# Kernel tuning notes

Measured on AMD Instinct MI355X. Metric: run time of the kernel, lower is better.

Reference implementation:

```python
import jax, jax.numpy as jnp
import numpy as np

NSAMPLE = 32
LAMBDA = 0.5


def setup_inputs() -> dict:
    key = jax.random.key(0)
    k1, k2, k3, k4, k5 = jax.random.split(key, 5)
    B, N, NPOINT, C, NCOMP = 4, 8192, 2048, 64, 16
    xyz = jax.random.normal(k1, (B, N, 3), dtype=jnp.float32)
    new_xyz = jax.random.normal(k2, (B, NPOINT, 3), dtype=jnp.float32)
    components = jax.random.randint(k3, (B, N, 1), 0, NCOMP, dtype=jnp.int64)
    new_components = jax.random.randint(k4, (B, NPOINT, 1), 0, NCOMP, dtype=jnp.int64)
    features = jax.random.normal(k5, (B, C, N), dtype=jnp.float32)
    return {"xyz": xyz, "new_xyz": new_xyz, "components": components,
            "new_components": new_components, "features": features}


def _gag_knn(new_xyz, xyz, new_comp, comp, k, lam):
    # squared pairwise distances (B, npoint, N), same math as sum((src-dst)**2)
    diff = new_xyz[:, :, None, :] - xyz[:, None, :, :]
    dists = jnp.sum(diff * diff, axis=-1)
    # component-aware rescale
    mask = comp[:, None, :] == new_comp[:, :, None]  # (B, npoint, N)
    dists = jnp.where(mask, dists * lam, dists * (1.0 - lam))
    # full argsort then take first k (faithful to original)
    idx = jnp.argsort(dists, axis=-1)[:, :, :k]  # (B, npoint, k)
    return idx.astype(jnp.int32)


def reference(xyz, new_xyz, components, new_components, features):
    comp = components[..., 0]
    new_comp = new_components[..., 0]
    idx = _gag_knn(new_xyz, xyz, new_comp, comp, NSAMPLE, LAMBDA)  # (B, npoint, ns)

    # group xyz: gather along N -> (B, npoint, ns, 3)
    grouped_xyz = jnp.take_along_axis(xyz[:, None, :, :], idx[..., None], axis=2)
    grouped_xyz = grouped_xyz - new_xyz[:, :, None, :]
    grouped_xyz = jnp.transpose(grouped_xyz, (0, 3, 1, 2))  # (B, 3, npoint, ns)

    # group features: (B, C, N) -> (B, npoint, ns, C) -> (B, C, npoint, ns)
    feats_bnc = jnp.transpose(features, (0, 2, 1))  # (B, N, C)
    grouped_feats = jnp.take_along_axis(feats_bnc[:, None, :, :], idx[..., None], axis=2)
    grouped_feats = jnp.transpose(grouped_feats, (0, 3, 1, 2))  # (B, C, npoint, ns)

    return jnp.concatenate([grouped_xyz, grouped_feats], axis=1)  # (B, 3+C, npoint, ns)
```

## Files before the change

kernel.cpp:

```cpp
#include <hip/hip_runtime.h>


#define BQ 4
#define NN_ 8192
#define NPOINT 2048
#define CF 64
#define NS 32
#define T1 256
#define PER (NN_ / T1)
#define CAP 1024

__global__ __launch_bounds__(256) void knn_kernel(const float* __restrict__ xyz,
                                                  const float* __restrict__ new_xyz,
                                                  int* __restrict__ idxOut) {
  const int q = blockIdx.x;
  const int b = q / NPOINT;
  const int tid = threadIdx.x;

  const float qx = new_xyz[q * 3 + 0];
  const float qy = new_xyz[q * 3 + 1];
  const float qz = new_xyz[q * 3 + 2];

  const float* __restrict__ base = xyz + (size_t)b * NN_ * 3;

  float d[PER];
  float lmin = 3.4e38f;
  int n = tid;
#pragma unroll
  for (int j = 0; j < PER; j++, n += T1) {
    float dx = base[n * 3 + 0] - qx;
    float dy = base[n * 3 + 1] - qy;
    float dz = base[n * 3 + 2] - qz;
    float dist = __fadd_rn(__fadd_rn(__fmul_rn(dx, dx), __fmul_rn(dy, dy)),
                           __fmul_rn(dz, dz));
    dist *= 0.5f;
    d[j] = dist;
    lmin = fminf(lmin, dist);
  }

  __shared__ float mins[T1];
  mins[tid] = lmin;
  __syncthreads();
  for (int k = 2; k <= T1; k <<= 1) {
    for (int j = k >> 1; j > 0; j >>= 1) {
      int ixj = tid ^ j;
      if (ixj > tid) {
        float a = mins[tid], bb = mins[ixj];
        bool up = ((tid & k) == 0);
        if (up ? (a > bb) : (a < bb)) { mins[tid] = bb; mins[ixj] = a; }
      }
      __syncthreads();
    }
  }
  const float theta = mins[NS - 1];

  __shared__ unsigned long long cand[CAP];
  __shared__ int cnt;
  if (tid == 0) cnt = 0;
  __syncthreads();
  n = tid;
#pragma unroll
  for (int j = 0; j < PER; j++, n += T1) {
    if (d[j] <= theta) {
      int pos = atomicAdd(&cnt, 1);
      if (pos < CAP)
        cand[pos] = ((unsigned long long)__float_as_uint(d[j]) << 32) | (unsigned)n;
    }
  }
  __syncthreads();
  int m = cnt < CAP ? cnt : CAP;

  for (int i = tid; i < m; i += T1) {
    unsigned long long x = cand[i];
    int r = 0;
    for (int j = 0; j < m; j++) r += (cand[j] < x) ? 1 : 0;
    if (r < NS) idxOut[q * NS + r] = (int)(x & 0xffffffffu);
  }
}

__global__ __launch_bounds__(256) void transpose_kernel(const float* __restrict__ f,
                                                        float* __restrict__ ft) {
  __shared__ float t[32][33];
  const int b = blockIdx.z;
  const int n0 = blockIdx.x * 32;
  const int c0 = blockIdx.y * 32;
  const int tx = threadIdx.x;
  const int ty = threadIdx.y;
#pragma unroll
  for (int i = 0; i < 4; i++) {
    int c = c0 + ty + i * 8;
    t[ty + i * 8][tx] = f[(size_t)b * CF * NN_ + (size_t)c * NN_ + n0 + tx];
  }
  __syncthreads();
#pragma unroll
  for (int i = 0; i < 4; i++) {
    int nrow = n0 + ty + i * 8;
    ft[(size_t)b * NN_ * CF + (size_t)nrow * CF + c0 + tx] = t[tx][ty + i * 8];
  }
}

#define FSTR 68
__global__ __launch_bounds__(256) void group_kernel(const float* __restrict__ xyz,
                                                    const float* __restrict__ new_xyz,
                                                    const float* __restrict__ featsT,
                                                    const int* __restrict__ idxArr,
                                                    float* __restrict__ out) {
  const int q = blockIdx.x;
  const int b = q / NPOINT;
  const int p = q - b * NPOINT;
  const int tid = threadIdx.x;

  __shared__ int sIdx[NS];
  __shared__ __align__(16) float ldsF[NS * FSTR];
  __shared__ float ldsX[3 * NS];

  if (tid < NS) sIdx[tid] = idxArr[q * NS + tid];
  __syncthreads();

  {
    int s = tid >> 3, r = tid & 7;
    int nn = sIdx[s];
    const float4* src = (const float4*)(featsT + ((size_t)b * NN_ + nn) * CF);
    float4 v0 = src[r * 2];
    float4 v1 = src[r * 2 + 1];
    float4* dst = (float4*)(ldsF + s * FSTR + r * 8);
    dst[0] = v0;
    dst[1] = v1;
  }
  if (tid < 96) {
    int dd = tid >> 5, s = tid & 31;
    int nn = sIdx[s];
    ldsX[dd * NS + s] = xyz[((size_t)b * NN_ + nn) * 3 + dd] -
                        new_xyz[(size_t)q * 3 + dd];
  }
  __syncthreads();

  const int s = tid & 31;
  const int r0 = tid >> 5;
#pragma unroll
  for (int k = 0; k < 9; k++) {
    int row = r0 + k * 8;
    if (row < 67) {
      float v = (row < 3) ? ldsX[row * NS + s] : ldsF[s * FSTR + (row - 3)];
      out[(((size_t)b * 67 + row) * NPOINT + p) * NS + s] = v;
    }
  }
}

extern "C" void kernel_launch(void* const* d_in, const int* in_sizes, int n_in,
                              void* d_out, int out_size, void* d_ws, size_t ws_size,
                              hipStream_t stream) {
  const float* xyz      = (const float*)d_in[0];
  const float* new_xyz  = (const float*)d_in[1];
  const float* features = (const float*)d_in[4];
  float* out = (float*)d_out;

  int* idxArr = (int*)d_ws;
  float* featsT = (float*)((char*)d_ws + (size_t)BQ * NPOINT * NS * sizeof(int));

  knn_kernel<<<BQ * NPOINT, T1, 0, stream>>>(xyz, new_xyz, idxArr);
  transpose_kernel<<<dim3(NN_ / 32, CF / 32, BQ), dim3(32, 8), 0, stream>>>(features, featsT);
  group_kernel<<<BQ * NPOINT, T1, 0, stream>>>(xyz, new_xyz, featsT, idxArr, out);
}
```

Measured before the change: 154.7 us.

## Use wavefront shuffle sort for kNN threshold and vectorize xyz loads

The 256-thread shared-memory bitonic sort, which needs a block barrier after every step, is replaced by a per-wavefront bitonic sort done with register shuffles. The threshold becomes the minimum over the four wavefronts of each wavefront's 32nd-smallest lane minimum. This bound is still valid but may be looser, so more candidates can enter the rank-selection phase. Each thread now also reads four consecutive points with three float4 loads instead of strided scalar loads, which is meant to improve global memory coalescing.

```diff
diff --git a/kernel.cpp b/kernel.cpp
--- a/kernel.cpp
+++ b/kernel.cpp
@@ -16,6 +16,8 @@
   const int q = blockIdx.x;
   const int b = q / NPOINT;
   const int tid = threadIdx.x;
+  const int lane = tid & 63;
+  const int wid = tid >> 6;
 
   const float qx = new_xyz[q * 3 + 0];
   const float qy = new_xyz[q * 3 + 1];
@@ -25,46 +27,62 @@
 
   float d[PER];
   float lmin = 3.4e38f;
-  int n = tid;
 #pragma unroll
-  for (int j = 0; j < PER; j++, n += T1) {
-    float dx = base[n * 3 + 0] - qx;
-    float dy = base[n * 3 + 1] - qy;
-    float dz = base[n * 3 + 2] - qz;
-    float dist = __fadd_rn(__fadd_rn(__fmul_rn(dx, dx), __fmul_rn(dy, dy)),
-                           __fmul_rn(dz, dz));
-    dist *= 0.5f;
-    d[j] = dist;
-    lmin = fminf(lmin, dist);
+  for (int j = 0; j < PER / 4; j++) {
+    const int n0 = j * 1024 + tid * 4;
+    const float4* p = (const float4*)(base + (size_t)n0 * 3);
+    float4 v0 = p[0];
+    float4 v1 = p[1];
+    float4 v2 = p[2];
+    float xs[4] = {v0.x, v0.w, v1.z, v2.y};
+    float ys[4] = {v0.y, v1.x, v1.w, v2.z};
+    float zs[4] = {v0.z, v1.y, v2.x, v2.w};
+#pragma unroll
+    for (int i = 0; i < 4; i++) {
+      float dx = xs[i] - qx;
+      float dy = ys[i] - qy;
+      float dz = zs[i] - qz;
+      float dist = __fadd_rn(__fadd_rn(__fmul_rn(dx, dx), __fmul_rn(dy, dy)),
+                             __fmul_rn(dz, dz));
+      dist *= 0.5f;
+      d[j * 4 + i] = dist;
+      lmin = fminf(lmin, dist);
+    }
   }
 
-  __shared__ float mins[T1];
-  mins[tid] = lmin;
-  __syncthreads();
-  for (int k = 2; k <= T1; k <<= 1) {
+  float v = lmin;
+#pragma unroll
+  for (int k = 2; k <= 64; k <<= 1) {
+#pragma unroll
     for (int j = k >> 1; j > 0; j >>= 1) {
-      int ixj = tid ^ j;
-      if (ixj > tid) {
-        float a = mins[tid], bb = mins[ixj];
-        bool up = ((tid & k) == 0);
-        if (up ? (a > bb) : (a < bb)) { mins[tid] = bb; mins[ixj] = a; }
-      }
-      __syncthreads();
+      float o = __shfl_xor(v, j);
+      bool up = ((lane & k) == 0);
+      bool lower = ((lane & j) == 0);
+      float mn = fminf(v, o), mx = fmaxf(v, o);
+      v = (up == lower) ? mn : mx;
     }
   }
-  const float theta = mins[NS - 1];
 
+  __shared__ float wTheta[4];
   __shared__ unsigned long long cand[CAP];
   __shared__ int cnt;
   if (tid == 0) cnt = 0;
+  if (lane == 31) wTheta[wid] = v;
   __syncthreads();
-  n = tid;
+  const float theta = fminf(fminf(wTheta[0], wTheta[1]),
+                            fminf(wTheta[2], wTheta[3]));
+
 #pragma unroll
-  for (int j = 0; j < PER; j++, n += T1) {
-    if (d[j] <= theta) {
-      int pos = atomicAdd(&cnt, 1);
-      if (pos < CAP)
-        cand[pos] = ((unsigned long long)__float_as_uint(d[j]) << 32) | (unsigned)n;
+  for (int j = 0; j < PER / 4; j++) {
+#pragma unroll
+    for (int i = 0; i < 4; i++) {
+      if (d[j * 4 + i] <= theta) {
+        int n = j * 1024 + tid * 4 + i;
+        int pos = atomicAdd(&cnt, 1);
+        if (pos < CAP)
+          cand[pos] = ((unsigned long long)__float_as_uint(d[j * 4 + i]) << 32) |
+                      (unsigned)n;
+      }
     }
   }
   __syncthreads();
```

After: 171.3 us. 10.7% more time.

## Batch four queries per block with expanded-norm distances and wave-level theta selection

Applied to the files above, without the earlier changes.

The KNN kernel now handles four query points per block, so each loaded xyz point is reused across four queries. Distances are computed as |p|^2 - 2p·q with a small epsilon margin, and the exact rounded distance is recomputed only for points that pass the threshold. The 256-element shared-memory bitonic sort with block-wide syncs is replaced by one 64-lane shuffle bitonic network per query wave, and candidate buffers shrink to 192 per query. In exchange the xyz data is read twice instead of being held in registers, and the expanded-norm threshold plus the smaller candidate cap risk overflow or ordering differences on edge cases.

```diff
diff --git a/kernel.cpp b/kernel.cpp
--- a/kernel.cpp
+++ b/kernel.cpp
@@ -8,73 +8,114 @@
 #define NS 32
 #define T1 256
 #define PER (NN_ / T1)
-#define CAP 1024
+#define QB 4
+#define CAPQ 192
+#define M_EPS 1e-3f
 
 __global__ __launch_bounds__(256) void knn_kernel(const float* __restrict__ xyz,
                                                   const float* __restrict__ new_xyz,
                                                   int* __restrict__ idxOut) {
-  const int q = blockIdx.x;
-  const int b = q / NPOINT;
+  const int tile = blockIdx.x;
+  const int b = tile / (NPOINT / QB);
+  const int q0 = b * NPOINT + (tile % (NPOINT / QB)) * QB;
   const int tid = threadIdx.x;
-
-  const float qx = new_xyz[q * 3 + 0];
-  const float qy = new_xyz[q * 3 + 1];
-  const float qz = new_xyz[q * 3 + 2];
+  const int lane = tid & 63;
+  const int wid = tid >> 6;
+
+  float qx[QB], qy[QB], qz[QB], qn[QB];
+#pragma unroll
+  for (int k = 0; k < QB; k++) {
+    qx[k] = new_xyz[(q0 + k) * 3 + 0];
+    qy[k] = new_xyz[(q0 + k) * 3 + 1];
+    qz[k] = new_xyz[(q0 + k) * 3 + 2];
+    qn[k] = qx[k] * qx[k] + qy[k] * qy[k] + qz[k] * qz[k];
+  }
 
   const float* __restrict__ base = xyz + (size_t)b * NN_ * 3;
 
-  float d[PER];
-  float lmin = 3.4e38f;
-  int n = tid;
-#pragma unroll
-  for (int j = 0; j < PER; j++, n += T1) {
-    float dx = base[n * 3 + 0] - qx;
-    float dy = base[n * 3 + 1] - qy;
-    float dz = base[n * 3 + 2] - qz;
-    float dist = __fadd_rn(__fadd_rn(__fmul_rn(dx, dx), __fmul_rn(dy, dy)),
-                           __fmul_rn(dz, dz));
-    dist *= 0.5f;
-    d[j] = dist;
-    lmin = fminf(lmin, dist);
-  }
-
-  __shared__ float mins[T1];
-  mins[tid] = lmin;
-  __syncthreads();
-  for (int k = 2; k <= T1; k <<= 1) {
-    for (int j = k >> 1; j > 0; j >>= 1) {
-      int ixj = tid ^ j;
-      if (ixj > tid) {
-        float a = mins[tid], bb = mins[ixj];
-        bool up = ((tid & k) == 0);
-        if (up ? (a > bb) : (a < bb)) { mins[tid] = bb; mins[ixj] = a; }
+  float smin_r[QB];
+#pragma unroll
+  for (int k = 0; k < QB; k++) smin_r[k] = 3.4e38f;
+
+  for (int j = 0; j < PER; j++) {
+    const int n = tid + j * T1;
+    const float x = base[n * 3 + 0];
+    const float y = base[n * 3 + 1];
+    const float z = base[n * 3 + 2];
+    const float pp = x * x + y * y + z * z;
+#pragma unroll
+    for (int k = 0; k < QB; k++) {
+      float dot = x * qx[k] + y * qy[k] + z * qz[k];
+      float s = pp - 2.0f * dot;
+      smin_r[k] = fminf(smin_r[k], s);
+    }
+  }
+
+  __shared__ float sMin[QB][T1];
+  __shared__ float sTheta[QB];
+  __shared__ unsigned long long cand[QB][CAPQ];
+  __shared__ int cnt[QB];
+#pragma unroll
+  for (int k = 0; k < QB; k++) sMin[k][tid] = smin_r[k];
+  if (tid < QB) cnt[tid] = 0;
+  __syncthreads();
+
+  {
+    const int k = wid;
+    float m = fminf(fminf(sMin[k][lane], sMin[k][lane + 64]),
+                    fminf(sMin[k][lane + 128], sMin[k][lane + 192]));
+#pragma unroll
+    for (int kk = 2; kk <= 64; kk <<= 1) {
+#pragma unroll
+      for (int jj = kk >> 1; jj > 0; jj >>= 1) {
+        float o = __shfl_xor(m, jj);
+        bool up = ((lane & kk) == 0);
+        bool lower = ((lane & jj) == 0);
+        m = (up == lower) ? fminf(m, o) : fmaxf(m, o);
       }
-      __syncthreads();
-    }
-  }
-  const float theta = mins[NS - 1];
-
-  __shared__ unsigned long long cand[CAP];
-  __shared__ int cnt;
-  if (tid == 0) cnt = 0;
-  __syncthreads();
-  n = tid;
-#pragma unroll
-  for (int j = 0; j < PER; j++, n += T1) {
-    if (d[j] <= theta) {
-      int pos = atomicAdd(&cnt, 1);
-      if (pos < CAP)
-        cand[pos] = ((unsigned long long)__float_as_uint(d[j]) << 32) | (unsigned)n;
-    }
-  }
-  __syncthreads();
-  int m = cnt < CAP ? cnt : CAP;
-
-  for (int i = tid; i < m; i += T1) {
-    unsigned long long x = cand[i];
-    int r = 0;
-    for (int j = 0; j < m; j++) r += (cand[j] < x) ? 1 : 0;
-    if (r < NS) idxOut[q * NS + r] = (int)(x & 0xffffffffu);
+    }
+    if (lane == 31) sTheta[k] = m + qn[k] + M_EPS;
+  }
+  __syncthreads();
+
+  float thd[QB];
+#pragma unroll
+  for (int k = 0; k < QB; k++) thd[k] = sTheta[k];
+
+  for (int j = 0; j < PER; j++) {
+    const int n = tid + j * T1;
+    const float x = base[n * 3 + 0];
+    const float y = base[n * 3 + 1];
+    const float z = base[n * 3 + 2];
+    const float pp = x * x + y * y + z * z;
+#pragma unroll
+    for (int k = 0; k < QB; k++) {
+      float dot = x * qx[k] + y * qy[k] + z * qz[k];
+      float s = pp - 2.0f * dot + qn[k];
+      if (s <= thd[k] + M_EPS) {
+        float dx = x - qx[k], dy = y - qy[k], dz = z - qz[k];
+        float d = __fadd_rn(__fadd_rn(__fmul_rn(dx, dx), __fmul_rn(dy, dy)),
+                            __fmul_rn(dz, dz));
+        if (d <= thd[k]) {
+          int pos = atomicAdd(&cnt[k], 1);
+          if (pos < CAPQ)
+            cand[k][pos] =
+                ((unsigned long long)__float_as_uint(d) << 32) | (unsigned)n;
+        }
+      }
+    }
+  }
+  __syncthreads();
+
+  {
+    const int k = wid;
+    const int m = cnt[k] < CAPQ ? cnt[k] : CAPQ;
+    for (int i = lane; i < m; i += 64) {
+      unsigned long long x = cand[k][i];
+      int r = 0;
+      for (int j = 0; j < m; j++) r += (cand[k][j] < x) ? 1 : 0;
+      if (r < NS) idxOut[(q0 + k) * NS + r] = (int)(x & 0xffffffffu);
+    }
   }
 }
 
@@ -158,7 +199,7 @@
   int* idxArr = (int*)d_ws;
   float* featsT = (float*)((char*)d_ws + (size_t)BQ * NPOINT * NS * sizeof(int));
 
-  knn_kernel<<<BQ * NPOINT, T1, 0, stream>>>(xyz, new_xyz, idxArr);
+  knn_kernel<<<BQ * NPOINT / QB, T1, 0, stream>>>(xyz, new_xyz, idxArr);
   transpose_kernel<<<dim3(NN_ / 32, CF / 32, BQ), dim3(32, 8), 0, stream>>>(features, featsT);
   group_kernel<<<BQ * NPOINT, T1, 0, stream>>>(xyz, new_xyz, featsT, idxArr, out);
 }
```

Result: faster. 147.1 us (-4.9%).
